# Optimization experiments

Measured on AMD Instinct MI355X. Metric: run time of the kernel, lower is better.

The kernel has to match this reference:

```python
import jax, jax.numpy as jnp
import numpy as np

P = 5.0
A = 10.0
NUM_VARS = 1_000_000
NUM_CLAUSES = 1_000_000
E = 3_000_000  # edges per polarity


def setup_inputs() -> dict:
    key = jax.random.key(0)
    k1, k2, k3, k4, k5 = jax.random.split(key, 5)
    xv = jax.random.uniform(k1, (NUM_VARS, 1), dtype=jnp.float32)
    # clause rows: shuffled arange % NUM_CLAUSES so every clause is non-empty
    cp = jax.random.permutation(k2, jnp.arange(E, dtype=jnp.int64) % NUM_CLAUSES)
    cn = jax.random.permutation(k3, jnp.arange(E, dtype=jnp.int64) % NUM_CLAUSES)
    vp = jax.random.randint(k4, (E,), 0, NUM_VARS, dtype=jnp.int64)
    vn = jax.random.randint(k5, (E,), 0, NUM_VARS, dtype=jnp.int64)
    adj_pos = jnp.stack([cp, vp])  # [2, E]
    adj_neg = jnp.stack([cn, vn])  # [2, E]
    clause_count = jnp.ones((NUM_CLAUSES,), dtype=jnp.float32)
    return {"xv": xv, "adj_pos": adj_pos, "adj_neg": adj_neg, "clause_count": clause_count}


def reference(xv, adj_pos, adj_neg, clause_count):
    x = xv.reshape(-1)            # [V]
    xn = 1.0 - x
    # gather literal values and their exp(p*.) weights along edges
    lit = jnp.concatenate([x[adj_pos[1]], xn[adj_neg[1]]])            # [2E]
    xe = jnp.concatenate([jnp.exp(P * x)[adj_pos[1]], jnp.exp(P * xn)[adj_neg[1]]])  # [2E]
    idx = jnp.concatenate([adj_pos[0], adj_neg[0]])                   # [2E]
    numerator = jax.ops.segment_sum(lit * xe, idx, num_segments=NUM_CLAUSES)
    dominator = jax.ops.segment_sum(xe, idx, num_segments=NUM_CLAUSES)
    # push_to_side: 1/(1+exp(a*(0.5-x))) == sigmoid(a*(x-0.5))
    sm = jax.nn.sigmoid(A * (numerator / dominator - 0.5))            # [NUM_CLAUSES]
    # metric = mse_loss(sm, clause_count)
    loss = jnp.mean((sm - clause_count) ** 2)
    return loss
```

## Files before the change

### kernel.cpp

```cpp
#include <hip/hip_runtime.h>

constexpr int   NUM_CLAUSES = 1000000;
constexpr int   NUM_EDGES   = 3000000;
constexpr float Pc = 5.0f;
constexpr float Ac = 10.0f;

constexpr float FXSCALE = 64.0f;
constexpr float FXINV   = 1.0f / 64.0f;

constexpr int NB  = 500;
constexpr int CPB = 2000;
constexpr int CAP = CPB * 6;

constexpr int TPB   = 1024;
constexpr int RPB   = 12288;
constexpr int RPT   = RPB / TPB;
constexpr int NBLKP = (NUM_EDGES + RPB - 1) / RPB;

constexpr float QSCALE = 1048575.0f;
constexpr float QINV   = 1.0f / 1048575.0f;

constexpr int CSTRIDE = 16;

constexpr size_t OFF_CTR = 24000000;
constexpr size_t OFF_PAR = OFF_CTR + (size_t)NB * CSTRIDE * 4;

__device__ __forceinline__ unsigned pack_fx(float num, float den) {
    unsigned lo = (unsigned)(num * FXSCALE + 0.5f);
    unsigned hi = (unsigned)(den * FXSCALE + 0.5f);
    return lo | (hi << 16);
}

__global__ __launch_bounds__(TPB, 8)
void partition_kernel(const int*   __restrict__ adj_pos,
                      const int*   __restrict__ adj_neg,
                      unsigned* __restrict__ recs,
                      unsigned* __restrict__ counters) {
    __shared__ unsigned       hist_sbase[NB];
    __shared__ unsigned       lbase[NB];
    __shared__ unsigned       srec[RPB];
    __shared__ unsigned short sbid[RPB];
    __shared__ unsigned       wsum[TPB / 64];
    __shared__ unsigned       woff[TPB / 64];

    const bool neg   = (blockIdx.x >= (unsigned)NBLKP);
    const int  sblk  = neg ? (int)blockIdx.x - NBLKP : (int)blockIdx.x;
    const int  start = sblk * RPB;
    const int  n     = min(RPB, NUM_EDGES - start);
    const int* crow  = neg ? adj_neg : adj_pos;
    const int* vrow  = crow + NUM_EDGES;
    const int  tid   = (int)threadIdx.x;
    const unsigned polbit = neg ? 0x800u : 0u;

    if (tid < NB) hist_sbase[tid] = 0;
    __syncthreads();

    int cc_[RPT], vv_[RPT];
    if (n == RPB) {
        #pragma unroll
        for (int j = 0; j < RPT / 4; ++j) {
            int4 c4 = ((const int4*)(crow + start))[j * TPB + tid];
            cc_[4*j] = c4.x; cc_[4*j+1] = c4.y; cc_[4*j+2] = c4.z; cc_[4*j+3] = c4.w;
        }
        #pragma unroll
        for (int j = 0; j < RPT / 4; ++j) {
            int4 v4 = ((const int4*)(vrow + start))[j * TPB + tid];
            vv_[4*j] = v4.x; vv_[4*j+1] = v4.y; vv_[4*j+2] = v4.z; vv_[4*j+3] = v4.w;
        }
    } else {
        #pragma unroll
        for (int r = 0; r < RPT; ++r) {
            int pos = 4 * ((r >> 2) * TPB + tid) + (r & 3);
            cc_[r] = (pos < n) ? crow[start + pos] : -1;
            vv_[r] = (pos < n) ? vrow[start + pos] : 0;
        }
    }

    unsigned meta[RPT];
    #pragma unroll
    for (int r = 0; r < RPT; ++r) {
        meta[r] = 0;
        if (cc_[r] >= 0) {
            int b = cc_[r] / CPB;
            unsigned rank = atomicAdd(&hist_sbase[b], 1u);
            meta[r] = ((unsigned)b << 14) | rank;
        }
    }
    __syncthreads();

    unsigned h    = (tid < NB) ? hist_sbase[tid] : 0u;
    unsigned incl = h;
    #pragma unroll
    for (int off = 1; off < 64; off <<= 1) {
        unsigned t = __shfl_up(incl, off, 64);
        if ((tid & 63) >= off) incl += t;
    }
    if ((tid & 63) == 63) wsum[tid >> 6] = incl;
    __syncthreads();
    if (tid == 0) {
        unsigned a = 0;
        #pragma unroll
        for (int w = 0; w < TPB / 64; ++w) { woff[w] = a; a += wsum[w]; }
    }
    __syncthreads();
    if (tid < NB) lbase[tid] = incl - h + woff[tid >> 6];
    __syncthreads();

    unsigned myres = 0;
    int      rb    = 0;
    if (tid < NB) {
        int boff = (int)blockIdx.x;
        while (boff >= NB) boff -= NB;
        rb = tid + boff;
        if (rb >= NB) rb -= NB;
        myres = atomicAdd(&counters[rb * CSTRIDE], hist_sbase[rb]);
    }

    #pragma unroll
    for (int r = 0; r < RPT; ++r) {
        if (cc_[r] >= 0) {
            unsigned b    = meta[r] >> 14;
            unsigned rank = meta[r] & 0x3FFFu;
            unsigned loc  = (unsigned)(cc_[r] - (int)b * CPB);
            unsigned p    = lbase[b] + rank;
            srec[p] = ((unsigned)vv_[r] << 12) | polbit | loc;
            sbid[p] = (unsigned short)b;
        }
    }
    if (tid < NB) hist_sbase[rb] = myres;
    __syncthreads();

    for (int p = tid; p < n; p += TPB) {
        unsigned b = sbid[p];
        recs[(size_t)b * CAP + hist_sbase[b] + ((unsigned)p - lbase[b])] = srec[p];
    }
}

__global__ __launch_bounds__(1024, 8)
void bucket_loss_kernel(const uint4* __restrict__ recs4,
                        const float* __restrict__ x,
                        const float* __restrict__ cc,
                        float* __restrict__ partials) {
    __shared__ unsigned lacc[CPB];
    const int b   = blockIdx.x;
    const int tid = (int)threadIdx.x;
    for (int j = tid; j < CPB; j += 1024) lacc[j] = 0;
    __syncthreads();

    const uint4* r4 = recs4 + (size_t)b * (CAP / 4);
    uint4 e0 = r4[tid];
    uint4 e1 = r4[tid + 1024];
    const bool has2 = (tid + 2048) < (CAP / 4);
    uint4 e2 = has2 ? r4[tid + 2048] : e0;

    float a0 = x[e0.x >> 12], a1 = x[e0.y >> 12], a2 = x[e0.z >> 12], a3 = x[e0.w >> 12];
    float b0 = x[e1.x >> 12], b1 = x[e1.y >> 12], b2 = x[e1.z >> 12], b3 = x[e1.w >> 12];
    float c0 = x[e2.x >> 12], c1 = x[e2.y >> 12], c2 = x[e2.z >> 12], c3 = x[e2.w >> 12];

    #define PROC(r, xv, act)                                               \
        do { if (act) {                                                    \
            float lit = ((r) & 0x800u) ? (1.0f - (xv)) : (xv);             \
            unsigned q = (unsigned)(lit * QSCALE + 0.5f);                  \
            float lq = (float)q * QINV;                                    \
            float w  = __expf(Pc * lq);                                    \
            atomicAdd(&lacc[(r) & 0x7FFu], pack_fx(lq * w, w));            \
        } } while (0)

    PROC(e0.x, a0, true); PROC(e0.y, a1, true); PROC(e0.z, a2, true); PROC(e0.w, a3, true);
    PROC(e1.x, b0, true); PROC(e1.y, b1, true); PROC(e1.z, b2, true); PROC(e1.w, b3, true);
    PROC(e2.x, c0, has2); PROC(e2.y, c1, has2); PROC(e2.z, c2, has2); PROC(e2.w, c3, has2);
    #undef PROC
    __syncthreads();

    float v = 0.0f;
    const float* gc = cc + (size_t)b * CPB;
    for (int j = tid; j < CPB; j += 1024) {
        unsigned a   = lacc[j];
        float    num = (float)(a & 0xffffu) * FXINV;
        float    den = (float)(a >> 16)     * FXINV;
        float    sm  = 1.0f / (1.0f + __expf(-Ac * (num / den - 0.5f)));
        float    e0f = sm - gc[j];
        v += e0f * e0f;
    }
    v *= 1.0f / (float)NUM_CLAUSES;

    #pragma unroll
    for (int off = 32; off > 0; off >>= 1)
        v += __shfl_down(v, off, 64);

    __shared__ float partial[16];
    int lane = tid & 63;
    int wid  = tid >> 6;
    if (lane == 0) partial[wid] = v;
    __syncthreads();
    if (tid == 0) {
        float s = 0.f;
        #pragma unroll
        for (int w = 0; w < 16; ++w) s += partial[w];
        partials[b] = s;
    }
}

__global__ void final_kernel(const float* __restrict__ partials,
                             float* __restrict__ out, int n) {
    float v = 0.0f;
    for (int i = threadIdx.x; i < n; i += 256) v += partials[i];

    #pragma unroll
    for (int off = 32; off > 0; off >>= 1)
        v += __shfl_down(v, off, 64);

    __shared__ float partial[4];
    int lane = threadIdx.x & 63;
    int wid  = threadIdx.x >> 6;
    if (lane == 0) partial[wid] = v;
    __syncthreads();
    if (threadIdx.x == 0)
        out[0] = partial[0] + partial[1] + partial[2] + partial[3];
}

extern "C" void kernel_launch(void* const* d_in, const int* in_sizes, int n_in,
                              void* d_out, int out_size, void* d_ws, size_t ws_size,
                              hipStream_t stream) {
    const float* xv      = (const float*)d_in[0];
    const int*   adj_pos = (const int*)  d_in[1];
    const int*   adj_neg = (const int*)  d_in[2];
    const float* cc      = (const float*)d_in[3];

    char* ws = (char*)d_ws;
    unsigned* recs     = (unsigned*)ws;
    unsigned* counters = (unsigned*)(ws + OFF_CTR);
    float*    partials = (float*)   (ws + OFF_PAR);
    float*    out      = (float*)d_out;

    hipMemsetAsync(counters, 0, (size_t)NB * CSTRIDE * sizeof(unsigned), stream);

    partition_kernel<<<2 * NBLKP, TPB, 0, stream>>>(adj_pos, adj_neg,
                                                    recs, counters);

    bucket_loss_kernel<<<NB, 1024, 0, stream>>>((const uint4*)recs, xv, cc,
                                                partials);

    final_kernel<<<1, 256, 0, stream>>>(partials, out, NB);
}
```

Baseline: 139.9 us.

## Shard bucket counters by superblock to cut global atomic contention

```diff
diff --git a/kernel.cpp b/kernel.cpp
--- a/kernel.cpp
+++ b/kernel.cpp
@@ -8,22 +8,25 @@
 constexpr float FXSCALE = 64.0f;
 constexpr float FXINV   = 1.0f / 64.0f;
 
+constexpr float QSCALE = 1048575.0f;
+constexpr float QINV   = 1.0f / 1048575.0f;
+
 constexpr int NB  = 500;
 constexpr int CPB = 2000;
-constexpr int CAP = CPB * 6;
 
 constexpr int TPB   = 1024;
 constexpr int RPB   = 12288;
 constexpr int RPT   = RPB / TPB;
 constexpr int NBLKP = (NUM_EDGES + RPB - 1) / RPB;
-
-constexpr float QSCALE = 1048575.0f;
-constexpr float QINV   = 1.0f / 1048575.0f;
-
-constexpr int CSTRIDE = 16;
-
-constexpr size_t OFF_CTR = 24000000;
-constexpr size_t OFF_PAR = OFF_CTR + (size_t)NB * CSTRIDE * 4;
+constexpr int NBLK  = 2 * NBLKP;
+
+constexpr int SBSH = 4;
+constexpr int NSB  = (NBLK + (1 << SBSH) - 1) >> SBSH;
+constexpr int CAPS = 544;
+
+
+constexpr size_t OFF_CTR = (size_t)NSB * NB * CAPS * 4;
+constexpr size_t OFF_PAR = OFF_CTR + (size_t)NSB * NB * 4;
 
 __device__ __forceinline__ unsigned pack_fx(float num, float den) {
     unsigned lo = (unsigned)(num * FXSCALE + 0.5f);
@@ -31,7 +34,7 @@
     return lo | (hi << 16);
 }
 
-__global__ __launch_bounds__(TPB, 8)
+__global__ __launch_bounds__(TPB)
 void partition_kernel(const int*   __restrict__ adj_pos,
                       const int*   __restrict__ adj_neg,
                       unsigned* __restrict__ recs,
@@ -45,6 +48,7 @@
 
     const bool neg   = (blockIdx.x >= (unsigned)NBLKP);
     const int  sblk  = neg ? (int)blockIdx.x - NBLKP : (int)blockIdx.x;
+    const int  sb    = (int)blockIdx.x >> SBSH;
     const int  start = sblk * RPB;
     const int  n     = min(RPB, NUM_EDGES - start);
     const int* crow  = neg ? adj_neg : adj_pos;
@@ -106,14 +110,14 @@
     if (tid < NB) lbase[tid] = incl - h + woff[tid >> 6];
     __syncthreads();
 
-    unsigned myres = 0;
+    unsigned gbase = 0;
     int      rb    = 0;
     if (tid < NB) {
-        int boff = (int)blockIdx.x;
-        while (boff >= NB) boff -= NB;
-        rb = tid + boff;
+        rb = tid + (int)blockIdx.x;
         if (rb >= NB) rb -= NB;
-        myres = atomicAdd(&counters[rb * CSTRIDE], hist_sbase[rb]);
+        unsigned hr   = hist_sbase[rb];
+        unsigned base = (unsigned)(sb * NB + rb) * (unsigned)CAPS;
+        gbase = base + (hr ? atomicAdd(&counters[sb * NB + rb], hr) : 0u);
     }
 
     #pragma unroll
@@ -127,49 +131,54 @@
             sbid[p] = (unsigned short)b;
         }
     }
-    if (tid < NB) hist_sbase[rb] = myres;
+    if (tid < NB) hist_sbase[rb] = gbase;
     __syncthreads();
 
     for (int p = tid; p < n; p += TPB) {
         unsigned b = sbid[p];
-        recs[(size_t)b * CAP + hist_sbase[b] + ((unsigned)p - lbase[b])] = srec[p];
-    }
-}
-
-__global__ __launch_bounds__(1024, 8)
-void bucket_loss_kernel(const uint4* __restrict__ recs4,
+        recs[hist_sbase[b] + ((unsigned)p - lbase[b])] = srec[p];
+    }
+}
+
+__global__ __launch_bounds__(1024)
+void bucket_loss_kernel(const unsigned* __restrict__ recs,
+                        const unsigned* __restrict__ counters,
                         const float* __restrict__ x,
                         const float* __restrict__ cc,
                         float* __restrict__ partials) {
     __shared__ unsigned lacc[CPB];
-    const int b   = blockIdx.x;
-    const int tid = (int)threadIdx.x;
+    const int b    = blockIdx.x;
+    const int tid  = (int)threadIdx.x;
+    const int lane = tid & 63;
+    const int wid  = tid >> 6;
     for (int j = tid; j < CPB; j += 1024) lacc[j] = 0;
     __syncthreads();
 
-    const uint4* r4 = recs4 + (size_t)b * (CAP / 4);
-    uint4 e0 = r4[tid];
-    uint4 e1 = r4[tid + 1024];
-    const bool has2 = (tid + 2048) < (CAP / 4);
-    uint4 e2 = has2 ? r4[tid + 2048] : e0;
-
-    float a0 = x[e0.x >> 12], a1 = x[e0.y >> 12], a2 = x[e0.z >> 12], a3 = x[e0.w >> 12];
-    float b0 = x[e1.x >> 12], b1 = x[e1.y >> 12], b2 = x[e1.z >> 12], b3 = x[e1.w >> 12];
-    float c0 = x[e2.x >> 12], c1 = x[e2.y >> 12], c2 = x[e2.z >> 12], c3 = x[e2.w >> 12];
-
-    #define PROC(r, xv, act)                                               \
-        do { if (act) {                                                    \
-            float lit = ((r) & 0x800u) ? (1.0f - (xv)) : (xv);             \
-            unsigned q = (unsigned)(lit * QSCALE + 0.5f);                  \
-            float lq = (float)q * QINV;                                    \
-            float w  = __expf(Pc * lq);                                    \
-            atomicAdd(&lacc[(r) & 0x7FFu], pack_fx(lq * w, w));            \
-        } } while (0)
-
-    PROC(e0.x, a0, true); PROC(e0.y, a1, true); PROC(e0.z, a2, true); PROC(e0.w, a3, true);
-    PROC(e1.x, b0, true); PROC(e1.y, b1, true); PROC(e1.z, b2, true); PROC(e1.w, b3, true);
-    PROC(e2.x, c0, has2); PROC(e2.y, c1, has2); PROC(e2.z, c2, has2); PROC(e2.w, c3, has2);
-    #undef PROC
+    for (int s = wid; s < NSB; s += 16) {
+        const unsigned idx = (unsigned)(s * NB + b);
+        const unsigned cnt = counters[idx];
+        const uint4*   rr  = (const uint4*)(recs + (size_t)idx * CAPS);
+        const int      nq  = (int)((cnt + 3u) >> 2);
+        for (int i = lane; i < nq; i += 64) {
+            uint4 e   = rr[i];
+            int   rem = (int)cnt - (i << 2);
+            #define PROC(r, act)                                           \
+                do { if (act) {                                            \
+                    unsigned rv  = (r);                                    \
+                    float    xv  = x[rv >> 12];                            \
+                    float    lit = (rv & 0x800u) ? (1.0f - xv) : xv;       \
+                    unsigned q   = (unsigned)(lit * QSCALE + 0.5f);        \
+                    float    lq  = (float)q * QINV;                        \
+                    float    w   = __expf(Pc * lq);                        \
+                    atomicAdd(&lacc[rv & 0x7FFu], pack_fx(lq * w, w));     \
+                } } while (0)
+            PROC(e.x, true);
+            PROC(e.y, rem > 1);
+            PROC(e.z, rem > 2);
+            PROC(e.w, rem > 3);
+            #undef PROC
+        }
+    }
     __syncthreads();
 
     float v = 0.0f;
@@ -189,8 +198,6 @@
         v += __shfl_down(v, off, 64);
 
     __shared__ float partial[16];
-    int lane = tid & 63;
-    int wid  = tid >> 6;
     if (lane == 0) partial[wid] = v;
     __syncthreads();
     if (tid == 0) {
@@ -233,12 +240,12 @@
     float*    partials = (float*)   (ws + OFF_PAR);
     float*    out      = (float*)d_out;
 
-    hipMemsetAsync(counters, 0, (size_t)NB * CSTRIDE * sizeof(unsigned), stream);
-
-    partition_kernel<<<2 * NBLKP, TPB, 0, stream>>>(adj_pos, adj_neg,
-                                                    recs, counters);
-
-    bucket_loss_kernel<<<NB, 1024, 0, stream>>>((const uint4*)recs, xv, cc,
+    hipMemsetAsync(counters, 0, (size_t)NSB * NB * sizeof(unsigned), stream);
+
+    partition_kernel<<<NBLK, TPB, 0, stream>>>(adj_pos, adj_neg,
+                                               recs, counters);
+
+    bucket_loss_kernel<<<NB, 1024, 0, stream>>>(recs, counters, xv, cc,
                                                 partials);
 
     final_kernel<<<1, 256, 0, stream>>>(partials, out, NB);
```

After: 137.8 us. No clear change (-1.5%).
